# Performance work log

Hardware: AMD Instinct MI355X
Metric: run time of the kernel (lower is better)

## Reference

```python
import jax, jax.numpy as jnp
import numpy as np

B, T, D, H = 2, 2048, 1024, 16
DK = D // H
NEG = -1e9  # stand-in for -inf; causal mask guarantees >=1 valid key per row


def setup_inputs() -> dict:
    key = jax.random.key(0)
    ks = jax.random.split(key, 9)
    s = 1.0 / np.sqrt(D)
    x = jax.random.normal(ks[0], (B, T, D), dtype=jnp.float32)
    mask = jnp.broadcast_to(jnp.tril(jnp.ones((T, T), dtype=jnp.int32))[None, None], (B, 1, T, T))
    params = {}
    for i, n in enumerate(['q', 'k', 'v', 'o']):
        params['W' + n] = jax.random.normal(ks[1 + 2 * i], (D, D), dtype=jnp.float32) * s
        params['b' + n] = jax.random.normal(ks[2 + 2 * i], (D,), dtype=jnp.float32) * s
    return dict(x=x, mask=mask, **params)


def reference(x, mask, Wq, bq, Wk, bk, Wv, bv, Wo, bo):
    Bx, Tx, Dx = x.shape
    # projections: [B,T,D] -> [B,H,T,DK]
    def split_heads(y):
        return y.reshape(Bx, Tx, H, DK).transpose(0, 2, 1, 3)
    Q = split_heads(x @ Wq + bq)
    K = split_heads(x @ Wk + bk)
    V = split_heads(x @ Wv + bv)
    scores = jnp.einsum('bhqd,bhkd->bhqk', Q, K) / jnp.sqrt(jnp.float32(DK))
    scores = jnp.where(mask == 0, NEG, scores)
    attn = jax.nn.softmax(scores, axis=-1)  # dropout is identity in eval / p=0
    out = jnp.einsum('bhqk,bhkd->bhqd', attn, V)
    out = out.transpose(0, 2, 1, 3).reshape(Bx, Tx, Dx)
    return out @ Wo + bo
```

## Files before the change

### kernel.cpp

```cpp
#include <hip/hip_runtime.h>
#include <hip/hip_bf16.h>

typedef __bf16 bf16;
typedef __attribute__((ext_vector_type(8))) __bf16 bf16x8;
typedef __attribute__((ext_vector_type(4))) __bf16 bf16x4;
typedef __attribute__((ext_vector_type(4))) float f32x4;

#define TSEQ 2048
#define DMODEL 1024
#define NHEAD 16
#define DKH 64
#define BATCH 2
#define NQKV 3072
#define PSTR 72

typedef __attribute__((address_space(1))) const void gv_t;
typedef __attribute__((address_space(3))) void sv_t;
__device__ __forceinline__ void gll16(const bf16* g, bf16* s) {
    __builtin_amdgcn_global_load_lds((gv_t*)g, (sv_t*)s, 16, 0, 0);
}
__device__ __forceinline__ void wait_vm0() {
    __builtin_amdgcn_s_waitcnt(0x0F70);
}

__global__ __launch_bounds__(256) void convert_bf16(
    const float* __restrict__ in, bf16* __restrict__ out)
{
    int i = (blockIdx.x * 256 + threadIdx.x) * 4;
    f32x4 v = *(const f32x4*)(in + i);
    bf16x4 o;
#pragma unroll
    for (int j = 0; j < 4; ++j) o[j] = (bf16)v[j];
    *(bf16x4*)(out + i) = o;
}

__global__ __launch_bounds__(256) void bias_concat(
    const float* __restrict__ bq, const float* __restrict__ bk,
    const float* __restrict__ bv, float* __restrict__ out)
{
    int i = blockIdx.x * 256 + threadIdx.x;
    float v = i < 1024 ? bq[i] : i < 2048 ? bk[i - 1024] : bv[i - 2048];
    out[i] = v;
}

__global__ __launch_bounds__(256) void transpose_w(
    const float* __restrict__ W0, const float* __restrict__ W1,
    const float* __restrict__ W2, const float* __restrict__ W3,
    bf16* __restrict__ WT)
{
    __shared__ float t[32][33];
    const float* W = blockIdx.z == 0 ? W0 : blockIdx.z == 1 ? W1
                   : blockIdx.z == 2 ? W2 : W3;
    bf16* T = WT + (size_t)blockIdx.z * DMODEL * DMODEL;
    int bx = blockIdx.x * 32, by = blockIdx.y * 32;
    int tx = threadIdx.x, ty = threadIdx.y;
#pragma unroll
    for (int i = 0; i < 4; ++i)
        t[ty + i * 8][tx] = W[(size_t)(by + ty + i * 8) * DMODEL + bx + tx];
    __syncthreads();
#pragma unroll
    for (int i = 0; i < 4; ++i)
        T[(size_t)(bx + ty + i * 8) * DMODEL + by + tx] = (bf16)t[tx][ty + i * 8];
}

__global__ __launch_bounds__(256) void transpose_v(
    const bf16* __restrict__ QKV, bf16* __restrict__ VT)
{
    __shared__ bf16 t[32][33];
    int b = blockIdx.z >> 4, h = blockIdx.z & 15;
    int t0 = blockIdx.x * 32, d0 = blockIdx.y * 32;
    int tx = threadIdx.x, ty = threadIdx.y;
#pragma unroll
    for (int i = 0; i < 4; ++i)
        t[ty + i * 8][tx] =
            QKV[(size_t)(b * TSEQ + t0 + ty + i * 8) * NQKV + 2048 + h * DKH + d0 + tx];
    __syncthreads();
#pragma unroll
    for (int i = 0; i < 4; ++i)
        VT[((size_t)(b * NHEAD + h) * DKH + d0 + ty + i * 8) * TSEQ + t0 + tx] =
            t[tx][ty + i * 8];
}

template <typename OutT>
__global__ __launch_bounds__(256) void gemm_bias_kernel(
    const bf16* __restrict__ A, const bf16* __restrict__ BT,
    const float* __restrict__ bias, OutT* __restrict__ C, int ldc)
{
    __shared__ bf16 As[128 * 32];
    __shared__ bf16 Bs[128 * 32];
    const int tid = threadIdx.x;
    const int ln = tid & 63, wave = tid >> 6;
    const int wm = wave >> 1, wn = wave & 1;
    const int lr = ln & 15, quad = ln >> 4;
    const int m0 = blockIdx.y * 128, n0 = blockIdx.x * 128;

    f32x4 acc[4][4] = {};

    const int grow = wave * 32 + (ln >> 2);
    const int gcol = (ln & 3) * 8;
    const bf16* Ag = A + (size_t)(m0 + grow) * DMODEL + gcol;
    const bf16* Bg = BT + (size_t)(n0 + grow) * DMODEL + gcol;
    bf16* AsW = As + wave * 1024;
    bf16* BsW = Bs + wave * 1024;

    for (int kt = 0; kt < DMODEL / 32; ++kt) {
        const int kk = kt * 32;
#pragma unroll
        for (int l = 0; l < 2; ++l) {
            gll16(Ag + (size_t)(l * 16) * DMODEL + kk, AsW + l * 512);
            gll16(Bg + (size_t)(l * 16) * DMODEL + kk, BsW + l * 512);
        }
        wait_vm0();
        __syncthreads();
        bf16x8 af[4], bfr[4];
#pragma unroll
        for (int i = 0; i < 4; ++i)
            af[i] = *(const bf16x8*)(As + (wm * 64 + i * 16 + lr) * 32 + quad * 8);
#pragma unroll
        for (int j = 0; j < 4; ++j)
            bfr[j] = *(const bf16x8*)(Bs + (wn * 64 + j * 16 + lr) * 32 + quad * 8);
#pragma unroll
        for (int i = 0; i < 4; ++i)
#pragma unroll
            for (int j = 0; j < 4; ++j)
                acc[i][j] = __builtin_amdgcn_mfma_f32_16x16x32_bf16(
                    af[i], bfr[j], acc[i][j], 0, 0, 0);
        __syncthreads();
    }

#pragma unroll
    for (int j = 0; j < 4; ++j) {
        int n = n0 + wn * 64 + j * 16 + lr;
        float bv = bias[n];
#pragma unroll
        for (int i = 0; i < 4; ++i) {
            int mb = m0 + wm * 64 + i * 16 + quad * 4;
#pragma unroll
            for (int r = 0; r < 4; ++r)
                C[(size_t)(mb + r) * ldc + n] = (OutT)(acc[i][j][r] + bv);
        }
    }
}

template <bool MASK>
__device__ __forceinline__ void attn_chunk(
    int kc, int q0w, int lr, int quad,
    const bf16* __restrict__ KsB, const bf16* __restrict__ VsB,
    bf16* __restrict__ Pw,
    const bf16x8 qb[2], f32x4 oacc[4], float& lrow)
{
    const int sw = lr & 7;
    bf16x8 kb[4][2];
#pragma unroll
    for (int kt = 0; kt < 4; ++kt)
#pragma unroll
        for (int kk = 0; kk < 2; ++kk)
            kb[kt][kk] = *(const bf16x8*)(KsB + (kt * 16 + lr) * 64 +
                                          (((kk * 4 + quad) ^ sw) * 8));
    f32x4 st[4] = {};
#pragma unroll
    for (int kt = 0; kt < 4; ++kt)
#pragma unroll
        for (int kk = 0; kk < 2; ++kk)
            st[kt] = __builtin_amdgcn_mfma_f32_16x16x32_bf16(
                kb[kt][kk], qb[kk], st[kt], 0, 0, 0);

    const float scale2 = 0.18033688f;
    const int q = q0w + lr;
    float rs = 0.f;
#pragma unroll
    for (int kt = 0; kt < 4; ++kt) {
        bf16x4 p4;
#pragma unroll
        for (int r = 0; r < 4; ++r) {
            float p = exp2f(fmaf(st[kt][r], scale2, -24.0f));
            if (MASK && (kc + kt * 16 + quad * 4 + r > q)) p = 0.f;
            rs += p;
            p4[r] = (bf16)p;
        }
        *(bf16x4*)(Pw + lr * PSTR + kt * 16 + quad * 4) = p4;
    }
    rs += __shfl_xor(rs, 16);
    rs += __shfl_xor(rs, 32);
    lrow += rs;

#pragma unroll
    for (int kk = 0; kk < 2; ++kk) {
        bf16x8 pa = *(const bf16x8*)(Pw + lr * PSTR + kk * 32 + quad * 8);
#pragma unroll
        for (int dt = 0; dt < 4; ++dt) {
            bf16x8 vb = *(const bf16x8*)(VsB + (dt * 16 + lr) * 64 +
                                         (((kk * 4 + quad) ^ sw) * 8));
            oacc[dt] = __builtin_amdgcn_mfma_f32_16x16x32_bf16(
                pa, vb, oacc[dt], 0, 0, 0);
        }
    }
}

__global__ __launch_bounds__(512) void flash_attn(
    const bf16* __restrict__ QKV, const bf16* __restrict__ VT,
    bf16* __restrict__ O)
{
    __shared__ bf16 Ks[2][64 * 64];
    __shared__ bf16 Vs[2][64 * 64];
    __shared__ bf16 Pl[8][16 * PSTR];
    const int tid = threadIdx.x;
    const int ln = tid & 63, w = tid >> 6;
    const int lr = ln & 15, quad = ln >> 4;
    const int h = blockIdx.y, b = blockIdx.z;

    int xb = blockIdx.x;
    if ((h ^ b) & 1) xb = (TSEQ / 128 - 1) - xb;
    const int q0 = xb * 128;
    const int q0w = q0 + w * 16;
    bf16* Pw = Pl[w];

    const bf16* Qb = QKV + (size_t)b * TSEQ * NQKV + h * DKH;
    const bf16* Kb = Qb + 1024;
    const bf16* VTb = VT + (size_t)(b * NHEAD + h) * DKH * TSEQ;

    const int srow = (w & 3) * 16 + (ln >> 3);
    const int scol = ((ln & 7) ^ ((ln >> 3) & 7)) * 8;
    const bool stK = (w < 4);

    auto stage = [&](int buf, int kc) {
        if (stK) {
            const bf16* g = Kb + (size_t)(kc + srow) * NQKV + scol;
            bf16* s = &Ks[buf][(w & 3) * 16 * 64];
#pragma unroll
            for (int l = 0; l < 2; ++l)
                gll16(g + (size_t)(l * 8) * NQKV, s + l * 8 * 64);
        } else {
            const bf16* g = VTb + (size_t)srow * TSEQ + kc + scol;
            bf16* s = &Vs[buf][(w & 3) * 16 * 64];
#pragma unroll
            for (int l = 0; l < 2; ++l)
                gll16(g + (size_t)(l * 8) * TSEQ, s + l * 8 * 64);
        }
    };

    bf16x8 qb[2];
#pragma unroll
    for (int kk = 0; kk < 2; ++kk)
        qb[kk] = *(const bf16x8*)(Qb + (size_t)(q0w + lr) * NQKV +
                                  kk * 32 + quad * 8);

    f32x4 oacc[4] = {};
    float lrow = 0.f;

    const int nch = (q0 + 128) >> 6;
    stage(0, 0);
    wait_vm0();
    __syncthreads();
    for (int c = 0; c < nch; ++c) {
        if (c + 1 < nch) stage((c + 1) & 1, (c + 1) * 64);
        const int kc = c * 64;
        if (kc <= q0w + 15) {
            if (kc + 63 <= q0w)
                attn_chunk<false>(kc, q0w, lr, quad, Ks[c & 1], Vs[c & 1], Pw,
                                  qb, oacc, lrow);
            else
                attn_chunk<true>(kc, q0w, lr, quad, Ks[c & 1], Vs[c & 1], Pw,
                                 qb, oacc, lrow);
        }
        wait_vm0();
        __syncthreads();
    }

#pragma unroll
    for (int r = 0; r < 4; ++r) {
        float inv = 1.0f / __shfl(lrow, quad * 4 + r);
        int row = q0w + quad * 4 + r;
#pragma unroll
        for (int dt = 0; dt < 4; ++dt)
            O[(size_t)(b * TSEQ + row) * DMODEL + h * DKH + dt * 16 + lr] =
                (bf16)(oacc[dt][r] * inv);
    }
}

extern "C" void kernel_launch(void* const* d_in, const int* in_sizes, int n_in,
                              void* d_out, int out_size, void* d_ws, size_t ws_size,
                              hipStream_t stream)
{
    const float* x  = (const float*)d_in[0];
    const float* Wq = (const float*)d_in[2];
    const float* bq = (const float*)d_in[3];
    const float* Wk = (const float*)d_in[4];
    const float* bk = (const float*)d_in[5];
    const float* Wv = (const float*)d_in[6];
    const float* bv = (const float*)d_in[7];
    const float* Wo = (const float*)d_in[8];
    const float* bo = (const float*)d_in[9];

    char* ws = (char*)d_ws;
    bf16* xb   = (bf16*)(ws);
    bf16* QKV  = (bf16*)(ws + (8u  << 20));
    bf16* VT   = (bf16*)(ws + (32u << 20));
    bf16* O    = (bf16*)(ws + (40u << 20));
    bf16* WT   = (bf16*)(ws + (48u << 20));
    float* wsBias = (float*)VT;

    const int NX = BATCH * TSEQ * DMODEL;
    convert_bf16<<<NX / (256 * 4), 256, 0, stream>>>(x, xb);

    dim3 tb(32, 8);
    transpose_w<<<dim3(32, 32, 4), tb, 0, stream>>>(Wq, Wk, Wv, Wo, WT);
    bias_concat<<<NQKV / 256, 256, 0, stream>>>(bq, bk, bv, wsBias);

    gemm_bias_kernel<bf16><<<dim3(NQKV / 128, 32), 256, 0, stream>>>(
        xb, WT, wsBias, QKV, NQKV);

    transpose_v<<<dim3(TSEQ / 32, DKH / 32, BATCH * NHEAD), tb, 0, stream>>>(QKV, VT);

    flash_attn<<<dim3(TSEQ / 128, NHEAD, BATCH), 512, 0, stream>>>(QKV, VT, O);

    gemm_bias_kernel<float><<<dim3(DMODEL / 128, 32), 256, 0, stream>>>(
        O, WT + 3u * (1u << 20), bo, (float*)d_out, DMODEL);
}
```

Measured before the change: 217.0 us.

## Double-buffer GEMM tiles, stage epilogue through LDS, narrow output-projection tiles

The GEMM kernel now double-buffers its A/B LDS tiles, issuing the next k-slice's global-to-LDS loads before computing on the current one, so load latency overlaps the MFMAs. The epilogue writes results through shared memory and then emits coalesced 16-byte stores instead of scattered scalar stores. The output projection uses a 128x64 tile with one wave per 32 rows, doubling its block count to improve occupancy on a grid that was small. The cost is more LDS per block and extra barriers in the epilogue.

```diff
diff --git a/kernel.cpp b/kernel.cpp
--- a/kernel.cpp
+++ b/kernel.cpp
@@ -81,63 +81,129 @@
             t[tx][ty + i * 8];
 }
 
-template <typename OutT>
+template <typename OutT, int NW_N>
 __global__ __launch_bounds__(256) void gemm_bias_kernel(
     const bf16* __restrict__ A, const bf16* __restrict__ BT,
     const float* __restrict__ bias, OutT* __restrict__ C, int ldc)
 {
-    __shared__ bf16 As[128 * 32];
-    __shared__ bf16 Bs[128 * 32];
+    constexpr int BN    = NW_N * 64;
+    constexpr int MW    = 4 / NW_N;
+    constexpr int WROWS = 128 / MW;
+    constexpr int FM    = WROWS / 16;
+    constexpr int ASZ   = 128 * 32;
+    constexpr int BSZ   = BN * 32;
+    constexpr int BNP   = BN + 4;
+    constexpr int EPI   = sizeof(OutT) == 2 ? 128 * BN : 64 * BNP * 2;
+    constexpr int SMEM  = (2 * ASZ + 2 * BSZ) > EPI ? (2 * ASZ + 2 * BSZ) : EPI;
+    __shared__ bf16 smem[SMEM];
+    bf16* As0 = smem;
+    bf16* Bs0 = smem + 2 * ASZ;
+
     const int tid = threadIdx.x;
     const int ln = tid & 63, wave = tid >> 6;
-    const int wm = wave >> 1, wn = wave & 1;
+    const int wm = NW_N == 2 ? (wave >> 1) : wave;
+    const int wn = NW_N == 2 ? (wave & 1) : 0;
     const int lr = ln & 15, quad = ln >> 4;
-    const int m0 = blockIdx.y * 128, n0 = blockIdx.x * 128;
-
-    f32x4 acc[4][4] = {};
-
-    const int grow = wave * 32 + (ln >> 2);
+    const int m0 = blockIdx.y * 128, n0 = blockIdx.x * BN;
+
+    f32x4 acc[FM][4] = {};
+
+    const int grow = ln >> 2;
     const int gcol = (ln & 3) * 8;
-    const bf16* Ag = A + (size_t)(m0 + grow) * DMODEL + gcol;
-    const bf16* Bg = BT + (size_t)(n0 + grow) * DMODEL + gcol;
-    bf16* AsW = As + wave * 1024;
-    bf16* BsW = Bs + wave * 1024;
-
-    for (int kt = 0; kt < DMODEL / 32; ++kt) {
-        const int kk = kt * 32;
-#pragma unroll
-        for (int l = 0; l < 2; ++l) {
-            gll16(Ag + (size_t)(l * 16) * DMODEL + kk, AsW + l * 512);
-            gll16(Bg + (size_t)(l * 16) * DMODEL + kk, BsW + l * 512);
-        }
-        wait_vm0();
-        __syncthreads();
-        bf16x8 af[4], bfr[4];
-#pragma unroll
-        for (int i = 0; i < 4; ++i)
-            af[i] = *(const bf16x8*)(As + (wm * 64 + i * 16 + lr) * 32 + quad * 8);
+    const bf16* Ag = A + (size_t)(m0 + wave * 32 + grow) * DMODEL + gcol;
+    const bf16* Bg = BT + (size_t)(n0 + (NW_N == 2 ? wave * 32 : wave * 16) + grow) * DMODEL + gcol;
+
+    auto stage = [&](int buf, int kk) {
+        bf16* AsW = As0 + buf * ASZ + wave * 1024;
+        gll16(Ag + kk, AsW);
+        gll16(Ag + (size_t)16 * DMODEL + kk, AsW + 512);
+        if constexpr (NW_N == 2) {
+            bf16* BsW = Bs0 + buf * BSZ + wave * 1024;
+            gll16(Bg + kk, BsW);
+            gll16(Bg + (size_t)16 * DMODEL + kk, BsW + 512);
+        } else {
+            gll16(Bg + kk, Bs0 + buf * BSZ + wave * 512);
+        }
+    };
+
+    constexpr int NT = DMODEL / 32;
+    stage(0, 0);
+    wait_vm0();
+    __syncthreads();
+    for (int kt = 0; kt < NT; ++kt) {
+        if (kt + 1 < NT) stage((kt + 1) & 1, (kt + 1) * 32);
+        const bf16* AsB = As0 + (kt & 1) * ASZ;
+        const bf16* BsB = Bs0 + (kt & 1) * BSZ;
+        bf16x8 af[FM], bfr[4];
+#pragma unroll
+        for (int i = 0; i < FM; ++i)
+            af[i] = *(const bf16x8*)(AsB + (wm * WROWS + i * 16 + lr) * 32 + quad * 8);
 #pragma unroll
         for (int j = 0; j < 4; ++j)
-            bfr[j] = *(const bf16x8*)(Bs + (wn * 64 + j * 16 + lr) * 32 + quad * 8);
-#pragma unroll
-        for (int i = 0; i < 4; ++i)
+            bfr[j] = *(const bf16x8*)(BsB + (wn * 64 + j * 16 + lr) * 32 + quad * 8);
+#pragma unroll
+        for (int i = 0; i < FM; ++i)
 #pragma unroll
             for (int j = 0; j < 4; ++j)
                 acc[i][j] = __builtin_amdgcn_mfma_f32_16x16x32_bf16(
                     af[i], bfr[j], acc[i][j], 0, 0, 0);
+        wait_vm0();
         __syncthreads();
     }
 
-#pragma unroll
-    for (int j = 0; j < 4; ++j) {
-        int n = n0 + wn * 64 + j * 16 + lr;
-        float bv = bias[n];
-#pragma unroll
-        for (int i = 0; i < 4; ++i) {
-            int mb = m0 + wm * 64 + i * 16 + quad * 4;
-#pragma unroll
-            for (int r = 0; r < 4; ++r)
-                C[(size_t)(mb + r) * ldc + n] = (OutT)(acc[i][j][r] + bv);
+    if constexpr (sizeof(OutT) == 2) {
+        bf16* Cs = smem;
+#pragma unroll
+        for (int j = 0; j < 4; ++j) {
+            int nl = wn * 64 + j * 16 + lr;
+            float bv = bias[n0 + nl];
+#pragma unroll
+            for (int i = 0; i < FM; ++i) {
+                int ml = wm * WROWS + i * 16 + quad * 4;
+#pragma unroll
+                for (int r = 0; r < 4; ++r)
+                    Cs[(ml + r) * BN + nl] = (bf16)(acc[i][j][r] + bv);
+            }
+        }
+        __syncthreads();
+        constexpr int LPR = BN / 8;
+        constexpr int RPP = 256 / LPR;
+        const int rr = tid / LPR, cc = (tid % LPR) * 8;
+#pragma unroll
+        for (int p = 0; p < 128 / RPP; ++p) {
+            int row = p * RPP + rr;
+            *(bf16x8*)(C + (size_t)(m0 + row) * ldc + n0 + cc) =
+                *(const bf16x8*)(Cs + row * BN + cc);
+        }
+    } else {
+        float* Cf = (float*)smem;
+#pragma unroll
+        for (int half = 0; half < 2; ++half) {
+            if (((wm * WROWS) >> 6) == half) {
+#pragma unroll
+                for (int j = 0; j < 4; ++j) {
+                    int nl = wn * 64 + j * 16 + lr;
+                    float bv = bias[n0 + nl];
+#pragma unroll
+                    for (int i = 0; i < FM; ++i) {
+                        int ml = wm * WROWS + i * 16 + quad * 4 - half * 64;
+#pragma unroll
+                        for (int r = 0; r < 4; ++r)
+                            Cf[(ml + r) * BNP + nl] = acc[i][j][r] + bv;
+                    }
+                }
+            }
+            __syncthreads();
+            constexpr int LPR = BN / 4;
+            constexpr int RPP = 256 / LPR;
+            const int rr = tid / LPR, cc = (tid % LPR) * 4;
+#pragma unroll
+            for (int p = 0; p < 64 / RPP; ++p) {
+                int row = p * RPP + rr;
+                *(f32x4*)(C + (size_t)(m0 + half * 64 + row) * ldc + n0 + cc) =
+                    *(const f32x4*)(Cf + row * BNP + cc);
+            }
+            __syncthreads();
         }
     }
 }
@@ -307,13 +373,13 @@
     transpose_w<<<dim3(32, 32, 4), tb, 0, stream>>>(Wq, Wk, Wv, Wo, WT);
     bias_concat<<<NQKV / 256, 256, 0, stream>>>(bq, bk, bv, wsBias);
 
-    gemm_bias_kernel<bf16><<<dim3(NQKV / 128, 32), 256, 0, stream>>>(
+    gemm_bias_kernel<bf16, 2><<<dim3(NQKV / 128, 32), 256, 0, stream>>>(
         xb, WT, wsBias, QKV, NQKV);
 
     transpose_v<<<dim3(TSEQ / 32, DKH / 32, BATCH * NHEAD), tb, 0, stream>>>(QKV, VT);
 
     flash_attn<<<dim3(TSEQ / 128, NHEAD, BATCH), 512, 0, stream>>>(QKV, VT, O);
 
-    gemm_bias_kernel<float><<<dim3(DMODEL / 128, 32), 256, 0, stream>>>(
+    gemm_bias_kernel<float, 1><<<dim3(DMODEL / 64, 32), 256, 0, stream>>>(
         O, WT + 3u * (1u << 20), bo, (float*)d_out, DMODEL);
 }
```

After: 218.0 us. No clear change (+0.5%).
